# Kernel optimization log

Measured on AMD Instinct MI355X. Metric: run time of the kernel, lower is better.

The kernel has to match this reference:

```python
import jax, jax.numpy as jnp
import numpy as np

N, D, P, R, T, K = 200000, 128, 4096, 4, 3, 16

def setup_inputs() -> dict:
    key = jax.random.key(0)
    ks = jax.random.split(key, 9)
    return {
        "node_embeds": jax.random.normal(ks[0], (N, D), jnp.float32),
        "node_pairs": jax.random.randint(ks[1], (P, 2), 0, N),
        "node_type_ids": jax.random.randint(ks[2], (N,), 0, T),
        "neighbor_idx": jax.random.randint(ks[3], (P, 2, R, K), 0, N),
        "delta_t": jax.random.uniform(ks[4], (P, 2, R, K), jnp.float32),
        "W_phi": jax.random.normal(ks[5], (T, D, D), jnp.float32) * 0.05,
        "W_zeta": jax.random.normal(ks[6], (2 * D,), jnp.float32) * 0.05,
        "W_beta_w": jax.random.normal(ks[7], (R, D, D), jnp.float32) * 0.05,
        "W_beta_b": jax.random.normal(ks[8], (R, D), jnp.float32) * 0.05,
    }

def reference(node_embeds, node_pairs, node_type_ids, neighbor_idx, delta_t,
              W_phi, W_zeta, W_beta_w, W_beta_b):
    n = node_embeds.shape[0]
    # per-node type-specific linear: compute all types then select (T small)
    H_all = jnp.einsum('nd,tde->tne', node_embeds, W_phi)        # [T,N,D]
    H = H_all[node_type_ids, jnp.arange(n)]                      # [N,D]
    # micro attention: e = W_zeta([h_n; h_s]) * exp(-dt), softmax over K neighbors
    zn, zs = W_zeta[:D], W_zeta[D:]
    h_n = H[neighbor_idx]                                        # [P,2,R,K,D]
    e_n = jnp.einsum('psrkd,d->psrk', h_n, zn)
    e_s = jnp.einsum('psd,d->ps', H[node_pairs], zs)             # [P,2]
    e = (e_n + e_s[:, :, None, None]) * jnp.exp(-delta_t)        # [P,2,R,K]
    alpha = jax.nn.softmax(e, axis=-1)
    # meso: attention-weighted aggregation per relation, then per-relation linear
    h_nei = node_embeds[neighbor_idx]                            # [P,2,R,K,D]
    h_agg = jnp.einsum('psrk,psrkd->psrd', alpha, h_nei)         # [P,2,R,D]
    h_beta = jnp.einsum('psrd,rde->psre', h_agg, W_beta_w) + W_beta_b
    # macro: average over both pair sides and relations, sigmoid combine
    x_tilde = h_beta.mean(axis=(1, 2))                           # [P,D]
    return jax.nn.sigmoid(x_tilde)
```

## Files before the change

### kernel.cpp

```cpp
#include <hip/hip_runtime.h>
#include <hip/hip_bf16.h>

#define NN 200000
#define D 128
#define P 4096
#define R 4
#define T 3
#define K 16

__device__ __forceinline__ float bf2f(unsigned int u) {
    union { unsigned int i; float f; } c;
    c.i = u << 16;
    return c.f;
}
__device__ __forceinline__ unsigned short f2bf(float x) {
    union { float f; unsigned int i; } c; c.f = x;
    unsigned int r = c.i + 0x7FFFu + ((c.i >> 16) & 1u);
    return (unsigned short)(r >> 16);
}
__device__ __forceinline__ float ldE(const void* p, size_t i, int f32) {
    return f32 ? ((const float*)p)[i] : bf2f(((const unsigned short*)p)[i]);
}
__device__ __forceinline__ void ld8(const void* p, size_t off, int f32, float* o) {
    if (f32) {
        const float* q = (const float*)p + off;
        float4 a = *(const float4*)q;
        float4 b = *(const float4*)(q + 4);
        o[0]=a.x; o[1]=a.y; o[2]=a.z; o[3]=a.w;
        o[4]=b.x; o[5]=b.y; o[6]=b.z; o[7]=b.w;
    } else {
        uint4 r = *(const uint4*)((const unsigned short*)p + off);
        o[0]=bf2f(r.x & 0xffffu); o[1]=bf2f(r.x >> 16);
        o[2]=bf2f(r.y & 0xffffu); o[3]=bf2f(r.y >> 16);
        o[4]=bf2f(r.z & 0xffffu); o[5]=bf2f(r.z >> 16);
        o[6]=bf2f(r.w & 0xffffu); o[7]=bf2f(r.w >> 16);
    }
}

__global__ void detect_dtype(const unsigned short* __restrict__ emb, int* __restrict__ flag) {
    int tid = threadIdx.x;
    int bad = 0;
    #pragma unroll
    for (int i = 0; i < 4; ++i) {
        unsigned short u = emb[(size_t)(tid * 4 + i) * 2 * 97];
        unsigned int e = (u >> 7) & 0xFFu;
        if (e >= 147u) bad = 1;
    }
    int any_bad = __any(bad);
    if (tid == 0) *flag = any_bad ? 1 : 0;
}

__global__ void precompute_vu(const void* __restrict__ W_phi,
                              const void* __restrict__ W_zeta,
                              const int* __restrict__ flag,
                              float* __restrict__ ws_v, float* __restrict__ ws_u) {
    const int f32 = *flag;
    const int t = blockIdx.x;
    const int d = threadIdx.x;
    const size_t rb = (size_t)(t * D + d) * D;
    float av = 0.f, au = 0.f;
    for (int e = 0; e < D; e += 8) {
        float w[8], zn[8], zs[8];
        ld8(W_phi, rb + e, f32, w);
        ld8(W_zeta, e, f32, zn);
        ld8(W_zeta, D + e, f32, zs);
        #pragma unroll
        for (int q = 0; q < 8; ++q) { av += w[q] * zn[q]; au += w[q] * zs[q]; }
    }
    ws_v[t * D + d] = av;
    ws_u[t * D + d] = au;
}

__global__ __launch_bounds__(256) void precompute_c(
    const void* __restrict__ emb, const int* __restrict__ types,
    const float* __restrict__ ws_v, const float* __restrict__ ws_u,
    const int* __restrict__ flag,
    float* __restrict__ c, float* __restrict__ c2)
{
    __shared__ float vsh[T * D], ush[T * D];
    const int f32 = *flag;
    const int tid = threadIdx.x;
    for (int i = tid; i < T * D; i += 256) { vsh[i] = ws_v[i]; ush[i] = ws_u[i]; }
    __syncthreads();
    const int w = tid >> 6, l = tid & 63;
    const int grp = l >> 4, ch = l & 15;
    const int n = blockIdx.x * 16 + w * 4 + grp;
    if (n >= NN) return;
    const int t = types[n];
    float rv[8]; ld8(emb, (size_t)n * D + ch * 8, f32, rv);
    const float* vp = vsh + t * D + ch * 8;
    const float* up = ush + t * D + ch * 8;
    float a = 0.f, b = 0.f;
    #pragma unroll
    for (int q = 0; q < 8; ++q) { a += rv[q] * vp[q]; b += rv[q] * up[q]; }
    #pragma unroll
    for (int off = 1; off <= 8; off <<= 1) {
        a += __shfl_xor(a, off, 64);
        b += __shfl_xor(b, off, 64);
    }
    if (ch == 0) { c[n] = a; c2[n] = b; }
}

__global__ __launch_bounds__(256, 4) void fused_kernel(
    const void* __restrict__ emb,
    const int* __restrict__ pairs,
    const int* __restrict__ nbr,
    const void* __restrict__ dlt,
    const void* __restrict__ W_beta_w,
    const void* __restrict__ W_beta_b,
    const float* __restrict__ c,
    const float* __restrict__ c2,
    const int* __restrict__ flag,
    void* __restrict__ out)
{
    __shared__ float esc[128];
    __shared__ __align__(16) float gbuf[4 * D];
    __shared__ __align__(16) float ybuf[4 * D];

    const int f32  = *flag;
    const int p    = blockIdx.x;
    const int tid  = threadIdx.x;
    const int w    = tid >> 6;
    const int l    = tid & 63;
    const int rsub = l >> 4;
    const int ch   = l & 15;
    const int base = p * 2 * R * K;

    int  nbv[8];
    uint4 rb[8];
    if (!f32) {
        const unsigned short* eu = (const unsigned short*)emb;
        #pragma unroll
        for (int i = 0; i < 8; ++i) {
            int jj = ((i >> 2) * 64) + w * 16 + (i & 3) * 4 + rsub;
            nbv[i] = nbr[base + jj];
        }
        #pragma unroll
        for (int i = 0; i < 8; ++i)
            rb[i] = *(const uint4*)(eu + (size_t)nbv[i] * D + ch * 8);
    }

    if (tid < 128) {
        int s  = tid >> 6;
        int nb = nbr[base + tid];
        float ce = c[nb];
        float cs = c2[pairs[p * 2 + s]];
        float dt = ldE(dlt, (size_t)base + tid, f32);
        esc[tid] = (ce + cs) * __expf(-dt);
    }
    __syncthreads();

    if (tid < 8) {
        float ev[K];
        float mx = -1e30f;
        #pragma unroll
        for (int k = 0; k < K; ++k) { ev[k] = esc[tid * K + k]; mx = fmaxf(mx, ev[k]); }
        float sum = 0.f;
        #pragma unroll
        for (int k = 0; k < K; ++k) { ev[k] = __expf(ev[k] - mx); sum += ev[k]; }
        float inv = 1.f / sum;
        #pragma unroll
        for (int k = 0; k < K; ++k) esc[tid * K + k] = ev[k] * inv;
    }
    __syncthreads();

    float acc[8] = {0.f,0.f,0.f,0.f,0.f,0.f,0.f,0.f};
    if (!f32) {
        float al[8];
        #pragma unroll
        for (int i = 0; i < 8; ++i) {
            int jj = ((i >> 2) * 64) + w * 16 + (i & 3) * 4 + rsub;
            al[i] = esc[jj];
        }
        #pragma unroll
        for (int i = 0; i < 8; ++i) {
            float a = al[i];
            acc[0] += a * bf2f(rb[i].x & 0xffffu); acc[1] += a * bf2f(rb[i].x >> 16);
            acc[2] += a * bf2f(rb[i].y & 0xffffu); acc[3] += a * bf2f(rb[i].y >> 16);
            acc[4] += a * bf2f(rb[i].z & 0xffffu); acc[5] += a * bf2f(rb[i].z >> 16);
            acc[6] += a * bf2f(rb[i].w & 0xffffu); acc[7] += a * bf2f(rb[i].w >> 16);
        }
    } else {
        #pragma unroll
        for (int i = 0; i < 8; ++i) {
            int jj = ((i >> 2) * 64) + w * 16 + (i & 3) * 4 + rsub;
            int nb = nbr[base + jj];
            float a = esc[jj];
            float rv[8]; ld8(emb, (size_t)nb * D + ch * 8, 1, rv);
            #pragma unroll
            for (int q = 0; q < 8; ++q) acc[q] += a * rv[q];
        }
    }
    #pragma unroll
    for (int q = 0; q < 8; ++q) {
        acc[q] += __shfl_xor(acc[q], 16, 64);
        acc[q] += __shfl_xor(acc[q], 32, 64);
    }
    if (rsub == 0) {
        *(float4*)(gbuf + w * D + ch * 8)     = make_float4(acc[0], acc[1], acc[2], acc[3]);
        *(float4*)(gbuf + w * D + ch * 8 + 4) = make_float4(acc[4], acc[5], acc[6], acc[7]);
    }
    __syncthreads();

    {
        const int dq = rsub;
        float y[8] = {0.f,0.f,0.f,0.f,0.f,0.f,0.f,0.f};
        #pragma unroll 4
        for (int dd = 0; dd < 32; ++dd) {
            int d = dq * 32 + dd;
            float gd = gbuf[w * D + d];
            float wb[8]; ld8(W_beta_w, ((size_t)(w * D + d)) * D + ch * 8, f32, wb);
            #pragma unroll
            for (int q = 0; q < 8; ++q) y[q] += gd * wb[q];
        }
        #pragma unroll
        for (int q = 0; q < 8; ++q) {
            y[q] += __shfl_xor(y[q], 16, 64);
            y[q] += __shfl_xor(y[q], 32, 64);
        }
        if (dq == 0) {
            *(float4*)(ybuf + w * D + ch * 8)     = make_float4(y[0], y[1], y[2], y[3]);
            *(float4*)(ybuf + w * D + ch * 8 + 4) = make_float4(y[4], y[5], y[6], y[7]);
        }
    }
    __syncthreads();

    if (tid < 128) {
        int e = tid;
        float x = ybuf[e] + ybuf[D + e] + ybuf[2 * D + e] + ybuf[3 * D + e];
        float bs = 0.f;
        #pragma unroll
        for (int r = 0; r < R; ++r) bs += ldE(W_beta_b, r * D + e, f32);
        x = (x + 2.f * bs) * 0.125f;
        float o = 1.f / (1.f + __expf(-x));
        size_t oi = (size_t)p * D + e;
        if (f32) ((float*)out)[oi] = o;
        else     ((unsigned short*)out)[oi] = f2bf(o);
    }
}

extern "C" void kernel_launch(void* const* d_in, const int* in_sizes, int n_in,
                              void* d_out, int out_size, void* d_ws, size_t ws_size,
                              hipStream_t stream) {
    const void* emb    = d_in[0];
    const int*  pairs  = (const int*)d_in[1];
    const int*  types  = (const int*)d_in[2];
    const int*  nbr    = (const int*)d_in[3];
    const void* dlt    = d_in[4];
    const void* W_phi  = d_in[5];
    const void* W_zeta = d_in[6];
    const void* W_bw   = d_in[7];
    const void* W_bb   = d_in[8];

    int*   flag = (int*)d_ws;
    float* ws_v = (float*)d_ws + 64;
    float* ws_u = ws_v + T * D;
    float* c    = (float*)d_ws + 1024;
    float* c2   = c + NN;

    detect_dtype<<<dim3(1), dim3(64), 0, stream>>>((const unsigned short*)emb, flag);
    precompute_vu<<<dim3(T), dim3(D), 0, stream>>>(W_phi, W_zeta, flag, ws_v, ws_u);
    precompute_c<<<dim3((NN + 15) / 16), dim3(256), 0, stream>>>(emb, types, ws_v, ws_u, flag, c, c2);
    fused_kernel<<<dim3(P), dim3(256), 0, stream>>>(emb, pairs, nbr, dlt,
                                                    W_bw, W_bb, c, c2, flag, d_out);
}
```

Measured before the change: 248.0 us.

## Map one pair per wavefront and process four nodes per thread in precompute

```diff
diff --git a/kernel.cpp b/kernel.cpp
--- a/kernel.cpp
+++ b/kernel.cpp
@@ -84,21 +84,31 @@
     __syncthreads();
     const int w = tid >> 6, l = tid & 63;
     const int grp = l >> 4, ch = l & 15;
-    const int n = blockIdx.x * 16 + w * 4 + grp;
-    if (n >= NN) return;
-    const int t = types[n];
-    float rv[8]; ld8(emb, (size_t)n * D + ch * 8, f32, rv);
-    const float* vp = vsh + t * D + ch * 8;
-    const float* up = ush + t * D + ch * 8;
-    float a = 0.f, b = 0.f;
-    #pragma unroll
-    for (int q = 0; q < 8; ++q) { a += rv[q] * vp[q]; b += rv[q] * up[q]; }
-    #pragma unroll
-    for (int off = 1; off <= 8; off <<= 1) {
-        a += __shfl_xor(a, off, 64);
-        b += __shfl_xor(b, off, 64);
-    }
-    if (ch == 0) { c[n] = a; c2[n] = b; }
+    const int nbase = blockIdx.x * 64 + w * 4 + grp;
+
+    int   tt[4];
+    float rv[4][8];
+    #pragma unroll
+    for (int it = 0; it < 4; ++it) {
+        int n = nbase + it * 16;
+        tt[it] = types[n];
+        ld8(emb, (size_t)n * D + ch * 8, f32, rv[it]);
+    }
+    #pragma unroll
+    for (int it = 0; it < 4; ++it) {
+        int n = nbase + it * 16;
+        const float* vp = vsh + tt[it] * D + ch * 8;
+        const float* up = ush + tt[it] * D + ch * 8;
+        float a = 0.f, b = 0.f;
+        #pragma unroll
+        for (int q = 0; q < 8; ++q) { a += rv[it][q] * vp[q]; b += rv[it][q] * up[q]; }
+        #pragma unroll
+        for (int off = 1; off <= 8; off <<= 1) {
+            a += __shfl_xor(a, off, 64);
+            b += __shfl_xor(b, off, 64);
+        }
+        if (ch == 0) { c[n] = a; c2[n] = b; }
+    }
 }
 
 __global__ __launch_bounds__(256, 4) void fused_kernel(
@@ -113,129 +123,130 @@
     const int* __restrict__ flag,
     void* __restrict__ out)
 {
-    __shared__ float esc[128];
-    __shared__ __align__(16) float gbuf[4 * D];
-    __shared__ __align__(16) float ybuf[4 * D];
-
     const int f32  = *flag;
-    const int p    = blockIdx.x;
     const int tid  = threadIdx.x;
-    const int w    = tid >> 6;
+    const int wv   = tid >> 6;
     const int l    = tid & 63;
+    const int p    = blockIdx.x * 4 + wv;
     const int rsub = l >> 4;
     const int ch   = l & 15;
     const int base = p * 2 * R * K;
 
-    int  nbv[8];
-    uint4 rb[8];
-    if (!f32) {
-        const unsigned short* eu = (const unsigned short*)emb;
-        #pragma unroll
-        for (int i = 0; i < 8; ++i) {
-            int jj = ((i >> 2) * 64) + w * 16 + (i & 3) * 4 + rsub;
-            nbv[i] = nbr[base + jj];
-        }
-        #pragma unroll
-        for (int i = 0; i < 8; ++i)
-            rb[i] = *(const uint4*)(eu + (size_t)nbv[i] * D + ch * 8);
-    }
-
-    if (tid < 128) {
-        int s  = tid >> 6;
-        int nb = nbr[base + tid];
-        float ce = c[nb];
-        float cs = c2[pairs[p * 2 + s]];
-        float dt = ldE(dlt, (size_t)base + tid, f32);
-        esc[tid] = (ce + cs) * __expf(-dt);
-    }
-    __syncthreads();
-
-    if (tid < 8) {
-        float ev[K];
-        float mx = -1e30f;
-        #pragma unroll
-        for (int k = 0; k < K; ++k) { ev[k] = esc[tid * K + k]; mx = fmaxf(mx, ev[k]); }
-        float sum = 0.f;
-        #pragma unroll
-        for (int k = 0; k < K; ++k) { ev[k] = __expf(ev[k] - mx); sum += ev[k]; }
-        float inv = 1.f / sum;
-        #pragma unroll
-        for (int k = 0; k < K; ++k) esc[tid * K + k] = ev[k] * inv;
-    }
-    __syncthreads();
-
-    float acc[8] = {0.f,0.f,0.f,0.f,0.f,0.f,0.f,0.f};
-    if (!f32) {
-        float al[8];
-        #pragma unroll
-        for (int i = 0; i < 8; ++i) {
-            int jj = ((i >> 2) * 64) + w * 16 + (i & 3) * 4 + rsub;
-            al[i] = esc[jj];
-        }
-        #pragma unroll
-        for (int i = 0; i < 8; ++i) {
-            float a = al[i];
-            acc[0] += a * bf2f(rb[i].x & 0xffffu); acc[1] += a * bf2f(rb[i].x >> 16);
-            acc[2] += a * bf2f(rb[i].y & 0xffffu); acc[3] += a * bf2f(rb[i].y >> 16);
-            acc[4] += a * bf2f(rb[i].z & 0xffffu); acc[5] += a * bf2f(rb[i].z >> 16);
-            acc[6] += a * bf2f(rb[i].w & 0xffffu); acc[7] += a * bf2f(rb[i].w >> 16);
-        }
-    } else {
-        #pragma unroll
-        for (int i = 0; i < 8; ++i) {
-            int jj = ((i >> 2) * 64) + w * 16 + (i & 3) * 4 + rsub;
-            int nb = nbr[base + jj];
-            float a = esc[jj];
-            float rv[8]; ld8(emb, (size_t)nb * D + ch * 8, 1, rv);
+    int nb0 = nbr[base + l];
+    int nb1 = nbr[base + 64 + l];
+    float cs0 = c2[pairs[p * 2]];
+    float cs1 = c2[pairs[p * 2 + 1]];
+    float dt0 = ldE(dlt, (size_t)base + l, f32);
+    float dt1 = ldE(dlt, (size_t)base + 64 + l, f32);
+    float e0 = (c[nb0] + cs0) * __expf(-dt0);
+    float e1 = (c[nb1] + cs1) * __expf(-dt1);
+
+    float m0 = e0, m1 = e1;
+    #pragma unroll
+    for (int off = 1; off <= 8; off <<= 1) {
+        m0 = fmaxf(m0, __shfl_xor(m0, off, 64));
+        m1 = fmaxf(m1, __shfl_xor(m1, off, 64));
+    }
+    float a0 = __expf(e0 - m0), a1 = __expf(e1 - m1);
+    float s0 = a0, s1 = a1;
+    #pragma unroll
+    for (int off = 1; off <= 8; off <<= 1) {
+        s0 += __shfl_xor(s0, off, 64);
+        s1 += __shfl_xor(s1, off, 64);
+    }
+    a0 *= (1.f / s0);
+    a1 *= (1.f / s1);
+
+    float y[8] = {0.f,0.f,0.f,0.f,0.f,0.f,0.f,0.f};
+    const unsigned short* eu = (const unsigned short*)emb;
+    const unsigned short* Wu = (const unsigned short*)W_beta_w;
+
+    #pragma unroll
+    for (int r = 0; r < R; ++r) {
+        float acc[8] = {0.f,0.f,0.f,0.f,0.f,0.f,0.f,0.f};
+        if (!f32) {
+            uint4 rbv[8]; float av[8];
             #pragma unroll
-            for (int q = 0; q < 8; ++q) acc[q] += a * rv[q];
-        }
-    }
+            for (int i = 0; i < 8; ++i) {
+                int srcl = r * 16 + (i & 3) * 4 + rsub;
+                int nb   = __shfl((i >> 2) ? nb1 : nb0, srcl, 64);
+                av[i]    = __shfl((i >> 2) ? a1  : a0,  srcl, 64);
+                rbv[i]   = *(const uint4*)(eu + (size_t)nb * D + ch * 8);
+            }
+            #pragma unroll
+            for (int i = 0; i < 8; ++i) {
+                float a = av[i];
+                acc[0] += a * bf2f(rbv[i].x & 0xffffu); acc[1] += a * bf2f(rbv[i].x >> 16);
+                acc[2] += a * bf2f(rbv[i].y & 0xffffu); acc[3] += a * bf2f(rbv[i].y >> 16);
+                acc[4] += a * bf2f(rbv[i].z & 0xffffu); acc[5] += a * bf2f(rbv[i].z >> 16);
+                acc[6] += a * bf2f(rbv[i].w & 0xffffu); acc[7] += a * bf2f(rbv[i].w >> 16);
+            }
+        } else {
+            #pragma unroll
+            for (int i = 0; i < 8; ++i) {
+                int srcl = r * 16 + (i & 3) * 4 + rsub;
+                int nb   = __shfl((i >> 2) ? nb1 : nb0, srcl, 64);
+                float a  = __shfl((i >> 2) ? a1  : a0,  srcl, 64);
+                float rv[8]; ld8(emb, (size_t)nb * D + ch * 8, 1, rv);
+                #pragma unroll
+                for (int q = 0; q < 8; ++q) acc[q] += a * rv[q];
+            }
+        }
+        #pragma unroll
+        for (int q = 0; q < 8; ++q) {
+            acc[q] += __shfl_xor(acc[q], 16, 64);
+            acc[q] += __shfl_xor(acc[q], 32, 64);
+        }
+        #pragma unroll
+        for (int dd = 0; dd < 32; ++dd) {
+            float gd = __shfl(acc[dd & 7], ((l & 48) >> 2) + (dd >> 3), 64);
+            size_t wo = ((size_t)(r * D + (rsub * 32 + dd))) * D + ch * 8;
+            if (!f32) {
+                uint4 wr = *(const uint4*)(Wu + wo);
+                y[0] += gd * bf2f(wr.x & 0xffffu); y[1] += gd * bf2f(wr.x >> 16);
+                y[2] += gd * bf2f(wr.y & 0xffffu); y[3] += gd * bf2f(wr.y >> 16);
+                y[4] += gd * bf2f(wr.z & 0xffffu); y[5] += gd * bf2f(wr.z >> 16);
+                y[6] += gd * bf2f(wr.w & 0xffffu); y[7] += gd * bf2f(wr.w >> 16);
+            } else {
+                float wb[8]; ld8(W_beta_w, wo, 1, wb);
+                #pragma unroll
+                for (int q = 0; q < 8; ++q) y[q] += gd * wb[q];
+            }
+        }
+    }
+
     #pragma unroll
     for (int q = 0; q < 8; ++q) {
-        acc[q] += __shfl_xor(acc[q], 16, 64);
-        acc[q] += __shfl_xor(acc[q], 32, 64);
+        y[q] += __shfl_xor(y[q], 16, 64);
+        y[q] += __shfl_xor(y[q], 32, 64);
+    }
+
+    float bs[8] = {0.f,0.f,0.f,0.f,0.f,0.f,0.f,0.f};
+    #pragma unroll
+    for (int r = 0; r < R; ++r) {
+        float bb[8]; ld8(W_beta_b, (size_t)r * D + ch * 8, f32, bb);
+        #pragma unroll
+        for (int q = 0; q < 8; ++q) bs[q] += bb[q];
     }
     if (rsub == 0) {
-        *(float4*)(gbuf + w * D + ch * 8)     = make_float4(acc[0], acc[1], acc[2], acc[3]);
-        *(float4*)(gbuf + w * D + ch * 8 + 4) = make_float4(acc[4], acc[5], acc[6], acc[7]);
-    }
-    __syncthreads();
-
-    {
-        const int dq = rsub;
-        float y[8] = {0.f,0.f,0.f,0.f,0.f,0.f,0.f,0.f};
-        #pragma unroll 4
-        for (int dd = 0; dd < 32; ++dd) {
-            int d = dq * 32 + dd;
-            float gd = gbuf[w * D + d];
-            float wb[8]; ld8(W_beta_w, ((size_t)(w * D + d)) * D + ch * 8, f32, wb);
-            #pragma unroll
-            for (int q = 0; q < 8; ++q) y[q] += gd * wb[q];
-        }
+        float o[8];
         #pragma unroll
         for (int q = 0; q < 8; ++q) {
-            y[q] += __shfl_xor(y[q], 16, 64);
-            y[q] += __shfl_xor(y[q], 32, 64);
-        }
-        if (dq == 0) {
-            *(float4*)(ybuf + w * D + ch * 8)     = make_float4(y[0], y[1], y[2], y[3]);
-            *(float4*)(ybuf + w * D + ch * 8 + 4) = make_float4(y[4], y[5], y[6], y[7]);
-        }
-    }
-    __syncthreads();
-
-    if (tid < 128) {
-        int e = tid;
-        float x = ybuf[e] + ybuf[D + e] + ybuf[2 * D + e] + ybuf[3 * D + e];
-        float bs = 0.f;
-        #pragma unroll
-        for (int r = 0; r < R; ++r) bs += ldE(W_beta_b, r * D + e, f32);
-        x = (x + 2.f * bs) * 0.125f;
-        float o = 1.f / (1.f + __expf(-x));
-        size_t oi = (size_t)p * D + e;
-        if (f32) ((float*)out)[oi] = o;
-        else     ((unsigned short*)out)[oi] = f2bf(o);
+            float x = (y[q] + 2.f * bs[q]) * 0.125f;
+            o[q] = 1.f / (1.f + __expf(-x));
+        }
+        size_t ob = (size_t)p * D + ch * 8;
+        if (f32) {
+            *(float4*)((float*)out + ob)     = make_float4(o[0], o[1], o[2], o[3]);
+            *(float4*)((float*)out + ob + 4) = make_float4(o[4], o[5], o[6], o[7]);
+        } else {
+            uint4 pk;
+            pk.x = (unsigned int)f2bf(o[0]) | ((unsigned int)f2bf(o[1]) << 16);
+            pk.y = (unsigned int)f2bf(o[2]) | ((unsigned int)f2bf(o[3]) << 16);
+            pk.z = (unsigned int)f2bf(o[4]) | ((unsigned int)f2bf(o[5]) << 16);
+            pk.w = (unsigned int)f2bf(o[6]) | ((unsigned int)f2bf(o[7]) << 16);
+            *(uint4*)((unsigned short*)out + ob) = pk;
+        }
     }
 }
 
@@ -260,7 +271,7 @@
 
     detect_dtype<<<dim3(1), dim3(64), 0, stream>>>((const unsigned short*)emb, flag);
     precompute_vu<<<dim3(T), dim3(D), 0, stream>>>(W_phi, W_zeta, flag, ws_v, ws_u);
-    precompute_c<<<dim3((NN + 15) / 16), dim3(256), 0, stream>>>(emb, types, ws_v, ws_u, flag, c, c2);
-    fused_kernel<<<dim3(P), dim3(256), 0, stream>>>(emb, pairs, nbr, dlt,
-                                                    W_bw, W_bb, c, c2, flag, d_out);
-}
+    precompute_c<<<dim3(NN / 64), dim3(256), 0, stream>>>(emb, types, ws_v, ws_u, flag, c, c2);
+    fused_kernel<<<dim3(P / 4), dim3(256), 0, stream>>>(emb, pairs, nbr, dlt,
+                                                        W_bw, W_bb, c, c2, flag, d_out);
+}
```

Result: slower. 294.4 us (+18.7%).
